# Performance work log

Hardware: AMD Instinct MI355X
Metric: run time of the kernel (lower is better)

## Reference

```python
import jax, jax.numpy as jnp
import numpy as np

B, T, CIN, H = 128, 512, 512, 256  # batch, time, conv-in channels, hidden
G = 4 * H  # LSTM gate width (i,f,g,o in PyTorch order)


def setup_inputs() -> dict:
    key = jax.random.key(0)
    ks = jax.random.split(key, 13)
    s = 0.05
    return {
        "x": jax.random.normal(ks[0], (B, CIN, T, 1), jnp.float32),
        "w1": jax.random.normal(ks[1], (H, CIN), jnp.float32) * s,  # 1x1 conv -> [out,in]
        "b1": jax.random.normal(ks[2], (H,), jnp.float32) * s,
        "w2": jax.random.normal(ks[3], (H, H), jnp.float32) * s,
        "b2": jax.random.normal(ks[4], (H,), jnp.float32) * s,
        "w_ih_f": jax.random.normal(ks[5], (G, H), jnp.float32) * s,
        "w_hh_f": jax.random.normal(ks[6], (G, H), jnp.float32) * s,
        "b_ih_f": jax.random.normal(ks[7], (G,), jnp.float32) * s,
        "b_hh_f": jax.random.normal(ks[8], (G,), jnp.float32) * s,
        "w_ih_b": jax.random.normal(ks[9], (G, H), jnp.float32) * s,
        "w_hh_b": jax.random.normal(ks[10], (G, H), jnp.float32) * s,
        "b_ih_b": jax.random.normal(ks[11], (G,), jnp.float32) * s,
        "b_hh_b": jax.random.normal(ks[12], (G,), jnp.float32) * s,
    }


def _lstm(xg, w_hh):
    """Run LSTM over time. xg: [B,T,4H] = x@w_ih.T + b_ih + b_hh (precomputed)."""
    h0 = jnp.zeros((xg.shape[0], w_hh.shape[1]), xg.dtype)

    def step(carry, g_in):
        h, c = carry
        g = g_in + h @ w_hh.T
        i, f, gg, o = jnp.split(g, 4, axis=-1)
        c = jax.nn.sigmoid(f) * c + jax.nn.sigmoid(i) * jnp.tanh(gg)
        h = jax.nn.sigmoid(o) * jnp.tanh(c)
        return (h, c), h

    _, hs = jax.lax.scan(step, (h0, h0), jnp.swapaxes(xg, 0, 1))  # [T,B,H]
    return jnp.swapaxes(hs, 0, 1)  # [B,T,H]


def reference(x, w1, b1, w2, b2, w_ih_f, w_hh_f, b_ih_f, b_hh_f,
              w_ih_b, w_hh_b, b_ih_b, b_hh_b):
    # 1x1 convs == per-pixel GEMMs
    y = jax.nn.relu(jnp.einsum('bchw,oc->bohw', x, w1) + b1[None, :, None, None])
    y = jax.nn.relu(jnp.einsum('bchw,oc->bohw', y, w2) + b2[None, :, None, None])
    # torch .view(B, H_dim, -1) on contiguous [B,256,T,1] -> [B,T,256] (row-major reinterpret)
    seq = y.reshape(y.shape[0], y.shape[2], -1)  # [B,T,256]
    # forward direction
    xg_f = jnp.einsum('btd,gd->btg', seq, w_ih_f) + b_ih_f + b_hh_f
    h_f = _lstm(xg_f, w_hh_f)
    # backward direction: reverse time, run, reverse back
    seq_r = seq[:, ::-1, :]
    xg_b = jnp.einsum('btd,gd->btg', seq_r, w_ih_b) + b_ih_b + b_hh_b
    h_b = _lstm(xg_b, w_hh_b)[:, ::-1, :]
    out = jnp.concatenate([h_f, h_b], axis=-1)  # [B,T,2H]
    # dropout is identity at inference; return last timestep
    return out[:, -1, :]
```

## Files before the change

### kernel.cpp

```cpp
#include <hip/hip_runtime.h>
#include <math.h>

#define BATCH 128
#define TT 512
#define CIN 512
#define HID 256
#define GG 1024

typedef _Float16 half2_t __attribute__((ext_vector_type(2)));
typedef _Float16 half8_t __attribute__((ext_vector_type(8)));
typedef float f32x4_t __attribute__((ext_vector_type(4)));

__device__ __forceinline__ float sigf(float x) { return 1.f / (1.f + __expf(-x)); }
__device__ __forceinline__ float tanhf_(float x) {
    float a = fabsf(x);
    float e = __expf(-2.f * a);
    float r = (1.f - e) / (1.f + e);
    return copysignf(r, x);
}
__device__ __forceinline__ float fdot2_(half2_t a, half2_t b, float c) {
#if __has_builtin(__builtin_amdgcn_fdot2)
    return __builtin_amdgcn_fdot2(a, b, c, false);
#else
    return c + (float)a.x * (float)b.x + (float)a.y * (float)b.y;
#endif
}

__global__ void prep_cast(const float* __restrict__ w1, const float* __restrict__ w2,
                          const float* __restrict__ wih, const float* __restrict__ bih,
                          const float* __restrict__ bhh,
                          _Float16* __restrict__ w1h, _Float16* __restrict__ w2h,
                          _Float16* __restrict__ wihh, float* __restrict__ bsum)
{
    const int i = blockIdx.x * 256 + threadIdx.x;
    if (i < 131072) w1h[i] = (_Float16)w1[i];
    if (i < 65536)  w2h[i] = (_Float16)w2[i];
    if (i < 262144) wihh[i] = (_Float16)wih[i];
    if (i < 1024)   bsum[i] = bih[i] + bhh[i];
}

__global__ __launch_bounds__(256) void cast_transpose_x(
    const float* __restrict__ x, _Float16* __restrict__ xt)
{
    const int b = blockIdx.z, c0 = blockIdx.y * 64, t0 = blockIdx.x * 64;
    __shared__ float tl[64][68];
    const float* xb = x + (size_t)b * CIN * TT;
    const int tid = threadIdx.x;
    const int lt = (tid & 15) * 4, lc = tid >> 4;
    #pragma unroll
    for (int r = 0; r < 4; ++r) {
        const int c = lc + r * 16;
        float4 v = *(const float4*)(xb + (size_t)(c0 + c) * TT + t0 + lt);
        tl[c][lt] = v.x; tl[c][lt + 1] = v.y; tl[c][lt + 2] = v.z; tl[c][lt + 3] = v.w;
    }
    __syncthreads();
    const int trow = tid >> 2, coff = (tid & 3) * 16;
    _Float16 o[16];
    #pragma unroll
    for (int i = 0; i < 16; ++i) o[i] = (_Float16)tl[coff + i][trow];
    _Float16* dst = xt + (size_t)b * TT * CIN + (size_t)(t0 + trow) * CIN + c0 + coff;
    *(float4*)dst = *(float4*)&o[0];
    *(float4*)(dst + 8) = *(float4*)&o[8];
}

template <int RELU, int BIASROW>
__global__ __launch_bounds__(256, 4) void mfma_nt(
    const _Float16* __restrict__ A, const _Float16* __restrict__ B,
    const float* __restrict__ bias, _Float16* __restrict__ C,
    int M, int N, int K, long sA, long sB, long sC)
{
    __shared__ __align__(16) char smem[34816];
    _Float16 (*As)[40] = (_Float16(*)[40])smem;
    _Float16 (*Bs)[40] = (_Float16(*)[40])(smem + 10240);
    float (*Ct)[132] = (float(*)[132])smem;

    const int nb = blockIdx.z;
    A += (size_t)nb * sA; B += (size_t)nb * sB; C += (size_t)nb * sC;
    const int m0 = blockIdx.y * 128, n0 = blockIdx.x * 128;
    const int tid = threadIdx.x;
    const int wave = tid >> 6, lane = tid & 63;
    const int quad = lane >> 4, l15 = lane & 15;
    const int wm = (wave >> 1) * 64, wn = (wave & 1) * 64;
    const int srow = tid >> 1, sko = (tid & 1) * 16;

    f32x4_t acc[4][4];
    const f32x4_t zz = {0.f, 0.f, 0.f, 0.f};
    #pragma unroll
    for (int i = 0; i < 4; ++i)
        #pragma unroll
        for (int j = 0; j < 4; ++j) acc[i][j] = zz;

    for (int k0 = 0; k0 < K; k0 += 32) {
        {
            const float4* ga = (const float4*)(A + (size_t)(m0 + srow) * K + k0 + sko);
            float4 a0 = ga[0], a1 = ga[1];
            const float4* gb = (const float4*)(B + (size_t)(n0 + srow) * K + k0 + sko);
            float4 b0 = gb[0], b1 = gb[1];
            *(float4*)&As[srow][sko] = a0; *(float4*)&As[srow][sko + 8] = a1;
            *(float4*)&Bs[srow][sko] = b0; *(float4*)&Bs[srow][sko + 8] = b1;
        }
        __syncthreads();
        half8_t af[4], bf[4];
        #pragma unroll
        for (int i = 0; i < 4; ++i) af[i] = *(const half8_t*)&As[wm + i * 16 + l15][quad * 8];
        #pragma unroll
        for (int j = 0; j < 4; ++j) bf[j] = *(const half8_t*)&Bs[wn + j * 16 + l15][quad * 8];
        #pragma unroll
        for (int i = 0; i < 4; ++i)
            #pragma unroll
            for (int j = 0; j < 4; ++j)
                acc[i][j] = __builtin_amdgcn_mfma_f32_16x16x32_f16(af[i], bf[j], acc[i][j], 0, 0, 0);
        __syncthreads();
    }

    const int trow = tid >> 2, coff = (tid & 3) * 32;
    float bcol[32];
    if (!BIASROW) {
        #pragma unroll
        for (int i = 0; i < 8; ++i)
            *(float4*)&bcol[i * 4] = *(const float4*)&bias[n0 + coff + i * 4];
    }
    #pragma unroll
    for (int p = 0; p < 2; ++p) {
        if (p) __syncthreads();
        if ((wave >> 1) == p) {
            #pragma unroll
            for (int mi = 0; mi < 4; ++mi)
                #pragma unroll
                for (int ni = 0; ni < 4; ++ni)
                    #pragma unroll
                    for (int r = 0; r < 4; ++r)
                        Ct[mi * 16 + quad * 4 + r][wn + ni * 16 + l15] = acc[mi][ni][r];
        }
        __syncthreads();
        float brow = 0.f;
        if (BIASROW) brow = bias[m0 + p * 64 + trow];
        float vv[32];
        #pragma unroll
        for (int i = 0; i < 8; ++i) *(float4*)&vv[i * 4] = *(float4*)&Ct[trow][coff + i * 4];
        _Float16 o[32];
        #pragma unroll
        for (int i = 0; i < 32; ++i) {
            float v = vv[i] + (BIASROW ? brow : bcol[i]);
            if (RELU) v = fmaxf(v, 0.f);
            o[i] = (_Float16)v;
        }
        _Float16* dst = C + (size_t)(m0 + p * 64 + trow) * N + n0 + coff;
        #pragma unroll
        for (int i = 0; i < 4; ++i) *(float4*)(dst + i * 8) = *(float4*)&o[i * 8];
    }
}

__global__ __launch_bounds__(1024, 4) void lstm_scan7(
    const _Float16* __restrict__ xg, const float* __restrict__ whh,
    float* __restrict__ out)
{
    __shared__ __align__(16) _Float16 wlds[256 * 256];
    __shared__ __align__(16) float psh[4096];
    __shared__ __align__(16) _Float16 xgsh[2][1024];
    __shared__ __align__(16) _Float16 hshh[256];

    const int tid = threadIdx.x;
    const int b   = blockIdx.x;
    const int q4  = tid >> 8;
    const int s   = tid & 255;
    const _Float16* xgb = xg + (size_t)b * TT * GG;

    {
        const int sr = tid >> 2, c4 = tid & 3;
        const float* wr = whh + (size_t)(768 + sr) * 256;
        #pragma unroll
        for (int j = 0; j < 8; ++j) {
            const int g = c4 * 8 + j;
            const float4 w0 = *(const float4*)&wr[g * 8 + 0];
            const float4 w1 = *(const float4*)&wr[g * 8 + 4];
            float4 pk;
            half2_t* pp = (half2_t*)&pk;
            pp[0] = half2_t{(_Float16)w0.x, (_Float16)w0.y};
            pp[1] = half2_t{(_Float16)w0.z, (_Float16)w0.w};
            pp[2] = half2_t{(_Float16)w1.x, (_Float16)w1.y};
            pp[3] = half2_t{(_Float16)w1.z, (_Float16)w1.w};
            *(float4*)((char*)wlds + sr * 512 + ((g ^ (sr & 7)) << 4)) = pk;
        }
    }
    half2_t wI[32], wF[32], wGt[32];
    {
        const float4* pi = (const float4*)(whh + (size_t)(s)*256 + q4 * 64);
        const float4* pf = (const float4*)(whh + (size_t)(s + 256) * 256 + q4 * 64);
        const float4* pg = (const float4*)(whh + (size_t)(s + 512) * 256 + q4 * 64);
        #pragma unroll
        for (int k = 0; k < 16; ++k) {
            const float4 a = pi[k];
            wI[2 * k + 0] = half2_t{(_Float16)a.x, (_Float16)a.y};
            wI[2 * k + 1] = half2_t{(_Float16)a.z, (_Float16)a.w};
            const float4 f = pf[k];
            wF[2 * k + 0] = half2_t{(_Float16)f.x, (_Float16)f.y};
            wF[2 * k + 1] = half2_t{(_Float16)f.z, (_Float16)f.w};
            const float4 g = pg[k];
            wGt[2 * k + 0] = half2_t{(_Float16)g.x, (_Float16)g.y};
            wGt[2 * k + 1] = half2_t{(_Float16)g.z, (_Float16)g.w};
        }
    }
    if (tid < 128) ((unsigned int*)hshh)[tid] = 0u;
    if (q4 == 3) {
        *(uint2*)&xgsh[0][4 * s] = *(const uint2*)&xgb[4 * s];
    }
    float c = 0.f, hlast = 0.f;
    __syncthreads();

    const float4* hp = (const float4*)hshh + q4 * 8;
    const char* wob = (const char*)wlds + s * 512 + q4 * 128;
    const int sw3 = s & 7;

    for (int t = 0; t < TT; ++t) {
        if (q4 == 3 && t + 1 < TT) {
            *(uint2*)&xgsh[(t + 1) & 1][4 * s] =
                *(const uint2*)&xgb[(size_t)(t + 1) * GG + 4 * s];
        }
        float aI = 0.f, aF = 0.f, aG = 0.f, aO = 0.f;
        #pragma unroll
        for (int kk = 0; kk < 8; ++kk) {
            const float4 hv = hp[kk];
            const half2_t h0 = __builtin_bit_cast(half2_t, hv.x);
            const half2_t h1 = __builtin_bit_cast(half2_t, hv.y);
            const half2_t h2 = __builtin_bit_cast(half2_t, hv.z);
            const half2_t h3 = __builtin_bit_cast(half2_t, hv.w);
            const float4 wv = *(const float4*)(wob + ((kk ^ sw3) << 4));
            const half2_t o0 = __builtin_bit_cast(half2_t, wv.x);
            const half2_t o1 = __builtin_bit_cast(half2_t, wv.y);
            const half2_t o2 = __builtin_bit_cast(half2_t, wv.z);
            const half2_t o3 = __builtin_bit_cast(half2_t, wv.w);
            aI = fdot2_(wI[4 * kk + 0], h0, aI);
            aI = fdot2_(wI[4 * kk + 1], h1, aI);
            aI = fdot2_(wI[4 * kk + 2], h2, aI);
            aI = fdot2_(wI[4 * kk + 3], h3, aI);
            aF = fdot2_(wF[4 * kk + 0], h0, aF);
            aF = fdot2_(wF[4 * kk + 1], h1, aF);
            aF = fdot2_(wF[4 * kk + 2], h2, aF);
            aF = fdot2_(wF[4 * kk + 3], h3, aF);
            aG = fdot2_(wGt[4 * kk + 0], h0, aG);
            aG = fdot2_(wGt[4 * kk + 1], h1, aG);
            aG = fdot2_(wGt[4 * kk + 2], h2, aG);
            aG = fdot2_(wGt[4 * kk + 3], h3, aG);
            aO = fdot2_(o0, h0, aO);
            aO = fdot2_(o1, h1, aO);
            aO = fdot2_(o2, h2, aO);
            aO = fdot2_(o3, h3, aO);
        }
        psh[q4 * 1024 + s]       = aI;
        psh[q4 * 1024 + s + 256] = aF;
        psh[q4 * 1024 + s + 512] = aG;
        psh[q4 * 1024 + s + 768] = aO;
        __syncthreads();
        if (tid < 256) {
            const int cur = t & 1;
            const float gi = psh[s] + psh[1024 + s] + psh[2048 + s] + psh[3072 + s]
                             + (float)xgsh[cur][s];
            const float gf = psh[s + 256] + psh[1280 + s] + psh[2304 + s] + psh[3328 + s]
                             + (float)xgsh[cur][s + 256];
            const float gq = psh[s + 512] + psh[1536 + s] + psh[2560 + s] + psh[3584 + s]
                             + (float)xgsh[cur][s + 512];
            const float go = psh[s + 768] + psh[1792 + s] + psh[2816 + s] + psh[3840 + s]
                             + (float)xgsh[cur][s + 768];
            const float iv = sigf(gi), fv = sigf(gf), gv = tanhf_(gq), ov = sigf(go);
            c = fv * c + iv * gv;
            hlast = ov * tanhf_(c);
            hshh[s] = (_Float16)hlast;
        }
        __syncthreads();
    }
    if (tid < 256) out[(size_t)b * 512 + s] = hlast;
}

__global__ __launch_bounds__(256) void lstm_back_last(
    const _Float16* __restrict__ y2h, const float* __restrict__ wih,
    const float* __restrict__ bih, const float* __restrict__ bhh,
    float* __restrict__ out)
{
    const int b = blockIdx.x;
    const int t = threadIdx.x;
    __shared__ float s[256];
    s[t] = (float)y2h[(size_t)b * (HID * TT) + (TT - 1) * HID + t];
    __syncthreads();
    float acc[4];
    #pragma unroll
    for (int q = 0; q < 4; ++q) acc[q] = bih[t + q * 256] + bhh[t + q * 256];
    #pragma unroll
    for (int q = 0; q < 4; ++q) {
        const float* w = wih + (size_t)(t + q * 256) * 256;
        float a = acc[q];
        for (int k = 0; k < 256; k += 4) {
            const float4 w4 = *(const float4*)&w[k];
            const float4 h4 = *(const float4*)&s[k];
            a += w4.x * h4.x; a += w4.y * h4.y;
            a += w4.z * h4.z; a += w4.w * h4.w;
        }
        acc[q] = a;
    }
    const float i = sigf(acc[0]);
    const float g = tanhf_(acc[2]), o = sigf(acc[3]);
    const float c = i * g;
    const float h = o * tanhf_(c);
    out[(size_t)b * 512 + 256 + t] = h;
}

extern "C" void kernel_launch(void* const* d_in, const int* in_sizes, int n_in,
                              void* d_out, int out_size, void* d_ws, size_t ws_size,
                              hipStream_t stream) {
    const float* x      = (const float*)d_in[0];
    const float* w1     = (const float*)d_in[1];
    const float* b1     = (const float*)d_in[2];
    const float* w2     = (const float*)d_in[3];
    const float* b2     = (const float*)d_in[4];
    const float* w_ih_f = (const float*)d_in[5];
    const float* w_hh_f = (const float*)d_in[6];
    const float* b_ih_f = (const float*)d_in[7];
    const float* b_hh_f = (const float*)d_in[8];
    const float* w_ih_b = (const float*)d_in[9];
    const float* b_ih_b = (const float*)d_in[11];
    const float* b_hh_b = (const float*)d_in[12];
    float* out = (float*)d_out;

    char* ws = (char*)d_ws;
    _Float16* xgh  = (_Float16*)(ws);
    _Float16* xt   = (_Float16*)(ws + 134217728);
    _Float16* y1t  = (_Float16*)(ws + 201326592);
    _Float16* y2h  = (_Float16*)(ws + 234881024);
    _Float16* w1h  = (_Float16*)(ws + 268435456);
    _Float16* w2h  = (_Float16*)(ws + 268697600);
    _Float16* wihh = (_Float16*)(ws + 268828672);
    float*    bsum = (float*)   (ws + 269352960);

    prep_cast<<<1024, 256, 0, stream>>>(w1, w2, w_ih_f, b_ih_f, b_hh_f,
                                        w1h, w2h, wihh, bsum);
    cast_transpose_x<<<dim3(8, 8, BATCH), 256, 0, stream>>>(x, xt);
    mfma_nt<1, 0><<<dim3(2, 4, BATCH), 256, 0, stream>>>(
        xt, w1h, b1, y1t, 512, 256, 512, 512L * 512, 0, 512L * 256);
    mfma_nt<1, 1><<<dim3(4, 2, BATCH), 256, 0, stream>>>(
        w2h, y1t, b2, y2h, 256, 512, 256, 0, 512L * 256, 256L * 512);
    mfma_nt<0, 0><<<dim3(8, 512, 1), 256, 0, stream>>>(
        y2h, wihh, bsum, xgh, 65536, 1024, 256, 0, 0, 0);
    lstm_back_last<<<BATCH, 256, 0, stream>>>(y2h, w_ih_b, b_ih_b, b_hh_b, out);
    lstm_scan7<<<BATCH, 1024, 0, stream>>>(xgh, w_hh_f, out);
}
```

Baseline: 1.422 ms.

## Reduce LSTM gate partials with DPP quad shuffles and one barrier per step

Remaps the LSTM scan so the four threads of a quad handle one hidden unit's K-quarters and combine partial gate sums with DPP lane swaps instead of an LDS round trip. This removes the second barrier per timestep and the serial gate-finalisation phase run by only 256 threads. The output-gate weights now stream from a pre-permuted global fp16 buffer, relying on L1/L2, instead of living in LDS. The input-projection rows are interleaved by gate so each thread reads its own xg element directly. Every quad lane now computes the activations redundantly, and the O-weight reloads each step add memory traffic.

```diff
diff --git a/kernel.cpp b/kernel.cpp
--- a/kernel.cpp
+++ b/kernel.cpp
@@ -25,18 +25,37 @@
     return c + (float)a.x * (float)b.x + (float)a.y * (float)b.y;
 #endif
 }
+template <int CTRL>
+__device__ __forceinline__ float qadd(float v) {
+    int i = __builtin_bit_cast(int, v);
+    int j = __builtin_amdgcn_update_dpp(i, i, CTRL, 0xF, 0xF, true);
+    return v + __builtin_bit_cast(float, j);
+}
 
 __global__ void prep_cast(const float* __restrict__ w1, const float* __restrict__ w2,
                           const float* __restrict__ wih, const float* __restrict__ bih,
-                          const float* __restrict__ bhh,
+                          const float* __restrict__ bhh, const float* __restrict__ whh,
                           _Float16* __restrict__ w1h, _Float16* __restrict__ w2h,
-                          _Float16* __restrict__ wihh, float* __restrict__ bsum)
+                          _Float16* __restrict__ wihh, float* __restrict__ bsum,
+                          _Float16* __restrict__ wop)
 {
     const int i = blockIdx.x * 256 + threadIdx.x;
     if (i < 131072) w1h[i] = (_Float16)w1[i];
     if (i < 65536)  w2h[i] = (_Float16)w2[i];
-    if (i < 262144) wihh[i] = (_Float16)wih[i];
-    if (i < 1024)   bsum[i] = bih[i] + bhh[i];
+    if (i < 262144) {
+        const int r = i >> 8, col = i & 255;
+        const int j = r & 3, s = r >> 2;
+        wihh[i] = (_Float16)wih[(size_t)(j * 256 + s) * 256 + col];
+    }
+    if (i < 1024) {
+        const int j = i & 3, s = i >> 2;
+        bsum[i] = bih[j * 256 + s] + bhh[j * 256 + s];
+    }
+    if (i < 65536) {
+        const int e = i & 7, sq = (i >> 3) & 1023, kk = i >> 13;
+        const int s = sq >> 2, q4 = sq & 3;
+        wop[i] = (_Float16)whh[(size_t)(768 + s) * 256 + q4 * 64 + kk * 8 + e];
+    }
 }
 
 __global__ __launch_bounds__(256) void cast_transpose_x(
@@ -151,41 +170,20 @@
     }
 }
 
-__global__ __launch_bounds__(1024, 4) void lstm_scan7(
+__global__ __launch_bounds__(1024, 4) void lstm_scan8(
     const _Float16* __restrict__ xg, const float* __restrict__ whh,
-    float* __restrict__ out)
-{
-    __shared__ __align__(16) _Float16 wlds[256 * 256];
-    __shared__ __align__(16) float psh[4096];
-    __shared__ __align__(16) _Float16 xgsh[2][1024];
-    __shared__ __align__(16) _Float16 hshh[256];
+    const _Float16* __restrict__ wop, float* __restrict__ out)
+{
+    __shared__ __align__(16) _Float16 hsh[2][4][72];
 
     const int tid = threadIdx.x;
-    const int b   = blockIdx.x;
-    const int q4  = tid >> 8;
-    const int s   = tid & 255;
+    const int b = blockIdx.x;
+    const int s = tid >> 2, q4 = tid & 3;
     const _Float16* xgb = xg + (size_t)b * TT * GG;
 
+    half2_t wI[32], wF[32], wG[32];
     {
-        const int sr = tid >> 2, c4 = tid & 3;
-        const float* wr = whh + (size_t)(768 + sr) * 256;
-        #pragma unroll
-        for (int j = 0; j < 8; ++j) {
-            const int g = c4 * 8 + j;
-            const float4 w0 = *(const float4*)&wr[g * 8 + 0];
-            const float4 w1 = *(const float4*)&wr[g * 8 + 4];
-            float4 pk;
-            half2_t* pp = (half2_t*)&pk;
-            pp[0] = half2_t{(_Float16)w0.x, (_Float16)w0.y};
-            pp[1] = half2_t{(_Float16)w0.z, (_Float16)w0.w};
-            pp[2] = half2_t{(_Float16)w1.x, (_Float16)w1.y};
-            pp[3] = half2_t{(_Float16)w1.z, (_Float16)w1.w};
-            *(float4*)((char*)wlds + sr * 512 + ((g ^ (sr & 7)) << 4)) = pk;
-        }
-    }
-    half2_t wI[32], wF[32], wGt[32];
-    {
-        const float4* pi = (const float4*)(whh + (size_t)(s)*256 + q4 * 64);
+        const float4* pi = (const float4*)(whh + (size_t)s * 256 + q4 * 64);
         const float4* pf = (const float4*)(whh + (size_t)(s + 256) * 256 + q4 * 64);
         const float4* pg = (const float4*)(whh + (size_t)(s + 512) * 256 + q4 * 64);
         #pragma unroll
@@ -197,79 +195,86 @@
             wF[2 * k + 0] = half2_t{(_Float16)f.x, (_Float16)f.y};
             wF[2 * k + 1] = half2_t{(_Float16)f.z, (_Float16)f.w};
             const float4 g = pg[k];
-            wGt[2 * k + 0] = half2_t{(_Float16)g.x, (_Float16)g.y};
-            wGt[2 * k + 1] = half2_t{(_Float16)g.z, (_Float16)g.w};
-        }
-    }
-    if (tid < 128) ((unsigned int*)hshh)[tid] = 0u;
-    if (q4 == 3) {
-        *(uint2*)&xgsh[0][4 * s] = *(const uint2*)&xgb[4 * s];
-    }
-    float c = 0.f, hlast = 0.f;
+            wG[2 * k + 0] = half2_t{(_Float16)g.x, (_Float16)g.y};
+            wG[2 * k + 1] = half2_t{(_Float16)g.z, (_Float16)g.w};
+        }
+    }
+    if (tid < 288) ((unsigned int*)hsh)[tid] = 0u;
+    _Float16 xn = xgb[tid];
+    float c = 0.f, hv_out = 0.f;
     __syncthreads();
 
-    const float4* hp = (const float4*)hshh + q4 * 8;
-    const char* wob = (const char*)wlds + s * 512 + q4 * 128;
-    const int sw3 = s & 7;
-
+    unsigned long long wopa = (unsigned long long)(const char*)wop
+                            + (unsigned long long)tid * 16u;
     for (int t = 0; t < TT; ++t) {
-        if (q4 == 3 && t + 1 < TT) {
-            *(uint2*)&xgsh[(t + 1) & 1][4 * s] =
-                *(const uint2*)&xgb[(size_t)(t + 1) * GG + 4 * s];
-        }
-        float aI = 0.f, aF = 0.f, aG = 0.f, aO = 0.f;
-        #pragma unroll
-        for (int kk = 0; kk < 8; ++kk) {
-            const float4 hv = hp[kk];
-            const half2_t h0 = __builtin_bit_cast(half2_t, hv.x);
-            const half2_t h1 = __builtin_bit_cast(half2_t, hv.y);
-            const half2_t h2 = __builtin_bit_cast(half2_t, hv.z);
-            const half2_t h3 = __builtin_bit_cast(half2_t, hv.w);
-            const float4 wv = *(const float4*)(wob + ((kk ^ sw3) << 4));
-            const half2_t o0 = __builtin_bit_cast(half2_t, wv.x);
-            const half2_t o1 = __builtin_bit_cast(half2_t, wv.y);
-            const half2_t o2 = __builtin_bit_cast(half2_t, wv.z);
-            const half2_t o3 = __builtin_bit_cast(half2_t, wv.w);
-            aI = fdot2_(wI[4 * kk + 0], h0, aI);
-            aI = fdot2_(wI[4 * kk + 1], h1, aI);
-            aI = fdot2_(wI[4 * kk + 2], h2, aI);
-            aI = fdot2_(wI[4 * kk + 3], h3, aI);
-            aF = fdot2_(wF[4 * kk + 0], h0, aF);
-            aF = fdot2_(wF[4 * kk + 1], h1, aF);
-            aF = fdot2_(wF[4 * kk + 2], h2, aF);
-            aF = fdot2_(wF[4 * kk + 3], h3, aF);
-            aG = fdot2_(wGt[4 * kk + 0], h0, aG);
-            aG = fdot2_(wGt[4 * kk + 1], h1, aG);
-            aG = fdot2_(wGt[4 * kk + 2], h2, aG);
-            aG = fdot2_(wGt[4 * kk + 3], h3, aG);
-            aO = fdot2_(o0, h0, aO);
-            aO = fdot2_(o1, h1, aO);
-            aO = fdot2_(o2, h2, aO);
-            aO = fdot2_(o3, h3, aO);
-        }
-        psh[q4 * 1024 + s]       = aI;
-        psh[q4 * 1024 + s + 256] = aF;
-        psh[q4 * 1024 + s + 512] = aG;
-        psh[q4 * 1024 + s + 768] = aO;
+        asm volatile("" : "+v"(wopa));
+        const char* wopc = (const char*)wopa;
+        const int tn = (t + 1 < TT) ? t + 1 : t;
+        const _Float16 xn_next = xgb[(size_t)tn * GG + tid];
+
+        float aI0 = 0.f, aI1 = 0.f, aF0 = 0.f, aF1 = 0.f;
+        float aG0 = 0.f, aG1 = 0.f, aO0 = 0.f, aO1 = 0.f;
+        const float4* hp = (const float4*)&hsh[t & 1][q4][0];
+        #pragma unroll
+        for (int hh2 = 0; hh2 < 2; ++hh2) {
+            float4 olv[4];
+            #pragma unroll
+            for (int i2 = 0; i2 < 4; ++i2)
+                olv[i2] = *(const float4*)(wopc + (size_t)(hh2 * 4 + i2) * 16384);
+            #pragma unroll
+            for (int kk2 = 0; kk2 < 4; ++kk2) {
+                const int kk = hh2 * 4 + kk2;
+                const float4 hv = hp[kk];
+                const half2_t h0 = __builtin_bit_cast(half2_t, hv.x);
+                const half2_t h1 = __builtin_bit_cast(half2_t, hv.y);
+                const half2_t h2 = __builtin_bit_cast(half2_t, hv.z);
+                const half2_t h3 = __builtin_bit_cast(half2_t, hv.w);
+                aI0 = fdot2_(wI[4 * kk + 0], h0, aI0);
+                aF0 = fdot2_(wF[4 * kk + 0], h0, aF0);
+                aG0 = fdot2_(wG[4 * kk + 0], h0, aG0);
+                aI1 = fdot2_(wI[4 * kk + 1], h1, aI1);
+                aF1 = fdot2_(wF[4 * kk + 1], h1, aF1);
+                aG1 = fdot2_(wG[4 * kk + 1], h1, aG1);
+                aI0 = fdot2_(wI[4 * kk + 2], h2, aI0);
+                aF0 = fdot2_(wF[4 * kk + 2], h2, aF0);
+                aG0 = fdot2_(wG[4 * kk + 2], h2, aG0);
+                aI1 = fdot2_(wI[4 * kk + 3], h3, aI1);
+                aF1 = fdot2_(wF[4 * kk + 3], h3, aF1);
+                aG1 = fdot2_(wG[4 * kk + 3], h3, aG1);
+            }
+            #pragma unroll
+            for (int kk2 = 0; kk2 < 4; ++kk2) {
+                const int kk = hh2 * 4 + kk2;
+                const float4 hv = hp[kk];
+                const float4 wv = olv[kk2];
+                aO0 = fdot2_(__builtin_bit_cast(half2_t, wv.x),
+                             __builtin_bit_cast(half2_t, hv.x), aO0);
+                aO1 = fdot2_(__builtin_bit_cast(half2_t, wv.y),
+                             __builtin_bit_cast(half2_t, hv.y), aO1);
+                aO0 = fdot2_(__builtin_bit_cast(half2_t, wv.z),
+                             __builtin_bit_cast(half2_t, hv.z), aO0);
+                aO1 = fdot2_(__builtin_bit_cast(half2_t, wv.w),
+                             __builtin_bit_cast(half2_t, hv.w), aO1);
+            }
+        }
+        float aI = aI0 + aI1, aF = aF0 + aF1, aG = aG0 + aG1, aO = aO0 + aO1;
+        const float xv = (float)xn;
+        aI += (q4 == 0) ? xv : 0.f;
+        aF += (q4 == 1) ? xv : 0.f;
+        aG += (q4 == 2) ? xv : 0.f;
+        aO += (q4 == 3) ? xv : 0.f;
+        aI = qadd<0x4E>(qadd<0xB1>(aI));
+        aF = qadd<0x4E>(qadd<0xB1>(aF));
+        aG = qadd<0x4E>(qadd<0xB1>(aG));
+        aO = qadd<0x4E>(qadd<0xB1>(aO));
+        const float iv = sigf(aI), fv = sigf(aF), gv = tanhf_(aG), ov = sigf(aO);
+        c = fv * c + iv * gv;
+        hv_out = ov * tanhf_(c);
+        if (q4 == 0) hsh[(t + 1) & 1][s >> 6][s & 63] = (_Float16)hv_out;
+        xn = xn_next;
         __syncthreads();
-        if (tid < 256) {
-            const int cur = t & 1;
-            const float gi = psh[s] + psh[1024 + s] + psh[2048 + s] + psh[3072 + s]
-                             + (float)xgsh[cur][s];
-            const float gf = psh[s + 256] + psh[1280 + s] + psh[2304 + s] + psh[3328 + s]
-                             + (float)xgsh[cur][s + 256];
-            const float gq = psh[s + 512] + psh[1536 + s] + psh[2560 + s] + psh[3584 + s]
-                             + (float)xgsh[cur][s + 512];
-            const float go = psh[s + 768] + psh[1792 + s] + psh[2816 + s] + psh[3840 + s]
-                             + (float)xgsh[cur][s + 768];
-            const float iv = sigf(gi), fv = sigf(gf), gv = tanhf_(gq), ov = sigf(go);
-            c = fv * c + iv * gv;
-            hlast = ov * tanhf_(c);
-            hshh[s] = (_Float16)hlast;
-        }
-        __syncthreads();
-    }
-    if (tid < 256) out[(size_t)b * 512 + s] = hlast;
+    }
+    if (q4 == 0) out[(size_t)b * 512 + s] = hv_out;
 }
 
 __global__ __launch_bounds__(256) void lstm_back_last(
@@ -330,9 +335,10 @@
     _Float16* w2h  = (_Float16*)(ws + 268697600);
     _Float16* wihh = (_Float16*)(ws + 268828672);
     float*    bsum = (float*)   (ws + 269352960);
-
-    prep_cast<<<1024, 256, 0, stream>>>(w1, w2, w_ih_f, b_ih_f, b_hh_f,
-                                        w1h, w2h, wihh, bsum);
+    _Float16* wop  = (_Float16*)(ws + 269357056);
+
+    prep_cast<<<1024, 256, 0, stream>>>(w1, w2, w_ih_f, b_ih_f, b_hh_f, w_hh_f,
+                                        w1h, w2h, wihh, bsum, wop);
     cast_transpose_x<<<dim3(8, 8, BATCH), 256, 0, stream>>>(x, xt);
     mfma_nt<1, 0><<<dim3(2, 4, BATCH), 256, 0, stream>>>(
         xt, w1h, b1, y1t, 512, 256, 512, 512L * 512, 0, 512L * 256);
@@ -341,5 +347,5 @@
     mfma_nt<0, 0><<<dim3(8, 512, 1), 256, 0, stream>>>(
         y2h, wihh, bsum, xgh, 65536, 1024, 256, 0, 0, 0);
     lstm_back_last<<<BATCH, 256, 0, stream>>>(y2h, w_ih_b, b_ih_b, b_hh_b, out);
-    lstm_scan7<<<BATCH, 1024, 0, stream>>>(xgh, w_hh_f, out);
-}
+    lstm_scan8<<<BATCH, 1024, 0, stream>>>(xgh, w_hh_f, wop, out);
+}
```

After: 1.849 ms. 1.3x slower.
